# Kernel tuning notes

Hardware: AMD Instinct MI355X
Metric: run time of the kernel (lower is better)

Reference implementation:

```python
import jax, jax.numpy as jnp
import numpy as np

NUM_SCENES = 7
SHAPE = [512, 512, 256, 64]  # layer dims: 512->512->256->64
BATCH = 16384


def _xavier(key, shape):
    # nn.init.xavier_normal_ on (s, in, out): fan_in/fan_out from last two dims
    fan_in, fan_out = shape[-2], shape[-1]
    std = np.sqrt(2.0 / (fan_in + fan_out)).astype(np.float32)
    return jax.random.normal(key, shape, dtype=jnp.float32) * std


def setup_inputs() -> dict:
    key = jax.random.key(0)
    ks = jax.random.split(key, 16)
    inp = {
        "x": jax.random.normal(ks[0], (BATCH, SHAPE[0]), dtype=jnp.float32),
        "scene": jax.random.randint(ks[1], (BATCH,), 1, NUM_SCENES + 1, dtype=jnp.int64),
    }
    for i in range(3):
        din, dout = SHAPE[i], SHAPE[i + 1]
        inp[f"W{i}"] = _xavier(ks[2 + 4 * i], (NUM_SCENES, din, dout))
        inp[f"b{i}"] = jnp.zeros((NUM_SCENES, dout), dtype=jnp.float32)
        inp[f"gW{i}"] = _xavier(ks[3 + 4 * i], (1, din, dout))
        inp[f"gb{i}"] = jnp.zeros((1, dout), dtype=jnp.float32)
    return inp


def _star_linear(x, scene0, W, b, gW, gb, relu):
    # W: (S, in, out), gW: (1, in, out). Equivalent to gathering W[scene0]
    # and doing x[:,None,:] @ (w * gW), but computed as a dense GEMM over
    # all scenes followed by a per-sample select (avoids B*in*out gather).
    scaled = W * gW                                   # (S, in, out)
    out_all = jnp.einsum('bi,sio->bso', x, scaled)    # (B, S, out)
    out = jnp.take_along_axis(out_all, scene0[:, None, None], axis=1)[:, 0, :]
    out = out + b[scene0] + gb[0]
    if relu:
        out = jnp.maximum(out, 0.0)
    return out  # dropout is identity at eval


def reference(x, scene, W0, b0, gW0, gb0, W1, b1, gW1, gb1, W2, b2, gW2, gb2):
    scene0 = (scene - 1).astype(jnp.int32)
    h = _star_linear(x, scene0, W0, b0, gW0, gb0, relu=True)
    h = _star_linear(h, scene0, W1, b1, gW1, gb1, relu=True)
    h = _star_linear(h, scene0, W2, b2, gW2, gb2, relu=False)  # drop=True -> no relu
    return h
```

## Files before the change

kernel.cpp:

```cpp
#include <hip/hip_runtime.h>
#include <hip/hip_bf16.h>
#include <stdint.h>


#define BATCH   16384
#define NSCENE  7
#define TM      128
#define NBLK    (BATCH / 256)
#define MT_MAX  (BATCH / TM + NSCENE)
#define PADMAX  (BATCH + NSCENE * TM)

typedef __bf16 bf16x8 __attribute__((ext_vector_type(8)));
typedef float  f32x4  __attribute__((ext_vector_type(4)));

__device__ __forceinline__ ushort f2bf(float f) {
  union { float f; uint32_t u; } v; v.f = f;
  uint32_t r = (v.u + 0x7FFFu + ((v.u >> 16) & 1u)) >> 16;
  return (ushort)r;
}
__device__ __forceinline__ uint32_t pk2(float a, float b) {
  union { __hip_bfloat162 h; uint32_t u; } cv;
  cv.h = __float22bfloat162_rn(make_float2(a, b));
  return cv.u;
}
__device__ __forceinline__ void async16(const void* g, void* lds) {
  __builtin_amdgcn_global_load_lds(
      (const __attribute__((address_space(1))) uint32_t*)g,
      (__attribute__((address_space(3))) uint32_t*)lds, 16, 0, 0);
}

__device__ __forceinline__ void st_tile(const float* __restrict__ W,
                                        const float* __restrict__ gW,
                                        ushort* __restrict__ sT,
                                        int K, int N, int s, int n0, int k0,
                                        int tid) {
  __shared__ float tl[32][33];
  int tx = tid & 31, ty = tid >> 5;
  const float* Wp = W + (size_t)s * K * N;
#pragma unroll
  for (int i = 0; i < 4; i++) {
    int k = k0 + ty + i * 8;
    tl[ty + i * 8][tx] = Wp[(size_t)k * N + n0 + tx] * gW[(size_t)k * N + n0 + tx];
  }
  __syncthreads();
#pragma unroll
  for (int i = 0; i < 4; i++) {
    int n = n0 + ty + i * 8;
    sT[((size_t)s * N + n) * K + k0 + tx] = f2bf(tl[tx][ty + i * 8]);
  }
}

#define NB_W0 (16 * 16 * 7)
#define NB_W1 (8 * 16 * 7)
#define NB_W2 (2 * 8 * 7)
#define NB_BIAS 23
#define NB_CNT NBLK

__global__ __launch_bounds__(256) void prep_k(
    const float* __restrict__ W0, const float* __restrict__ gW0,
    const float* __restrict__ W1, const float* __restrict__ gW1,
    const float* __restrict__ W2, const float* __restrict__ gW2,
    const float* __restrict__ b0, const float* __restrict__ gb0,
    const float* __restrict__ b1, const float* __restrict__ gb1,
    const float* __restrict__ b2, const float* __restrict__ gb2,
    const int* __restrict__ scene,
    ushort* __restrict__ sT0, ushort* __restrict__ sT1, ushort* __restrict__ sT2,
    float* __restrict__ bias0, float* __restrict__ bias1, float* __restrict__ bias2,
    int* __restrict__ bcnt, int* __restrict__ rank) {
  int bid = blockIdx.x, tid = threadIdx.x;
  if (bid < NB_W0) {
    int l = bid;
    st_tile(W0, gW0, sT0, 512, 512, l / 256, (l % 16) * 32, ((l / 16) % 16) * 32, tid);
  } else if (bid < NB_W0 + NB_W1) {
    int l = bid - NB_W0;
    st_tile(W1, gW1, sT1, 512, 256, l / 128, (l % 8) * 32, ((l / 8) % 16) * 32, tid);
  } else if (bid < NB_W0 + NB_W1 + NB_W2) {
    int l = bid - NB_W0 - NB_W1;
    st_tile(W2, gW2, sT2, 256, 64, l / 16, (l % 2) * 32, ((l / 2) % 8) * 32, tid);
  } else if (bid < NB_W0 + NB_W1 + NB_W2 + NB_BIAS) {
    int t = (bid - NB_W0 - NB_W1 - NB_W2) * 256 + tid;
    if (t < 7 * 512) bias0[t] = b0[t] + gb0[t & 511];
    else if (t < 7 * 512 + 7 * 256) { int i = t - 7 * 512; bias1[i] = b1[i] + gb1[i & 255]; }
    else if (t < 7 * 512 + 7 * 256 + 7 * 64) { int i = t - 7 * 512 - 7 * 256; bias2[i] = b2[i] + gb2[i & 63]; }
  } else {
    __shared__ int l[NSCENE];
    if (tid < NSCENE) l[tid] = 0;
    __syncthreads();
    int blk = bid - NB_W0 - NB_W1 - NB_W2 - NB_BIAS;
    int i = blk * 256 + tid;
    int pos = atomicAdd(&l[scene[i] - 1], 1);
    rank[i] = pos;
    __syncthreads();
    if (tid < NSCENE) bcnt[blk * NSCENE + tid] = l[tid];
  }
}

#define PLAN_SHARED  __shared__ int sb[NBLK * NSCENE]; \
                     __shared__ int tot[NSCENE], padoff[NSCENE], cumt[NSCENE + 1];
__device__ __forceinline__ void plan_derive(const int* __restrict__ bcnt,
                                            int* sb, int* tot, int* padoff,
                                            int* cumt, int tid) {
  if (tid < NBLK * NSCENE) sb[tid] = bcnt[tid];
  if (tid + 256 < NBLK * NSCENE) sb[tid + 256] = bcnt[tid + 256];
  __syncthreads();
  if (tid < NSCENE) {
    int c = 0;
    for (int b = 0; b < NBLK; b++) c += sb[b * NSCENE + tid];
    tot[tid] = c;
  }
  __syncthreads();
  if (tid == 0) {
    int po = 0, ct = 0;
    for (int s = 0; s < NSCENE; s++) {
      padoff[s] = po; cumt[s] = ct;
      int tiles = (tot[s] + TM - 1) / TM;
      ct += tiles; po += tiles * TM;
    }
    cumt[NSCENE] = ct;
  }
  __syncthreads();
}

__global__ __launch_bounds__(256) void xc_k(const float* __restrict__ x,
                                            const int* __restrict__ scene,
                                            const int* __restrict__ rank,
                                            const int* __restrict__ bcnt,
                                            int* __restrict__ idxp,
                                            ushort* __restrict__ xc,
                                            int* __restrict__ plan_g) {
  PLAN_SHARED
  __shared__ int base7[NSCENE];
  int tid = threadIdx.x;
  plan_derive(bcnt, sb, tot, padoff, cumt, tid);
  if (blockIdx.x == 0) {
    if (tid < NSCENE) { plan_g[tid] = tot[tid]; plan_g[7 + tid] = padoff[tid]; }
    if (tid < NSCENE + 1) plan_g[14 + tid] = cumt[tid];
  }
  int myblk = blockIdx.x >> 5;
  if (tid < NSCENE) {
    int pre = 0;
    for (int b = 0; b < myblk; b++) pre += sb[b * NSCENE + tid];
    base7[tid] = padoff[tid] + pre;
  }
  __syncthreads();

  int r = blockIdx.x * 8 + (tid >> 5);
  int s = scene[r] - 1;
  int d = base7[s] + rank[r];
  if ((tid & 31) == 0) idxp[d] = r;
  int c = (tid & 31) * 16;
  const float4* p = (const float4*)(x + (size_t)r * 512 + c);
  float4 f0 = p[0], f1 = p[1], f2 = p[2], f3 = p[3];
  uint4 v0, v1;
  v0.x = pk2(f0.x, f0.y); v0.y = pk2(f0.z, f0.w);
  v0.z = pk2(f1.x, f1.y); v0.w = pk2(f1.z, f1.w);
  v1.x = pk2(f2.x, f2.y); v1.y = pk2(f2.z, f2.w);
  v1.z = pk2(f3.x, f3.y); v1.w = pk2(f3.z, f3.w);
  uint4* q = (uint4*)(xc + (size_t)d * 512 + c);
  q[0] = v0; q[1] = v1;
}

__global__ __launch_bounds__(256) void gemm0_k(
    const ushort* __restrict__ ain, const ushort* __restrict__ bw,
    const float* __restrict__ bias, const int* __restrict__ plan,
    ushort* __restrict__ hout) {
  __shared__ int splan[24];
  __shared__ __align__(16) ushort Abuf[128 * 64];
  __shared__ __align__(16) ushort Bbuf[128 * 64];

  int tid = threadIdx.x;
  if (tid < 22) splan[tid] = plan[tid];
  __syncthreads();
  const int* padoff = splan + 7;
  const int* cumt   = splan + 14;

  int t = blockIdx.x;
  if (t >= cumt[NSCENE]) return;
  int sc = 0;
  while (sc < NSCENE - 1 && t >= cumt[sc + 1]) sc++;
  int mrow0 = padoff[sc] + (t - cumt[sc]) * TM;
  int nb = blockIdx.y;

  int lane = tid & 63, wid = tid >> 6;
  int wr = wid >> 1, wc = wid & 1;

  f32x4 acc[4][4];
#pragma unroll
  for (int mt = 0; mt < 4; mt++)
#pragma unroll
    for (int nt = 0; nt < 4; nt++) acc[mt][nt] = (f32x4){0.f, 0.f, 0.f, 0.f};

  const ushort* bwS = bw + ((size_t)sc * 512 + (size_t)nb * 128) * 512;

  for (int kb = 0; kb < 8; kb++) {
#pragma unroll
    for (int i = 0; i < 4; i++) {
      int c = tid + i * 256;
      int row = c >> 3, q = c & 7;
      int kg = q ^ (row & 7);
      async16(ain + (size_t)(mrow0 + row) * 512 + kb * 64 + kg * 8,
              &Abuf[(size_t)(i * 256 + wid * 64) * 8]);
    }
#pragma unroll
    for (int i = 0; i < 4; i++) {
      int c = tid + i * 256;
      int row = c >> 3, q = c & 7;
      int kg = q ^ (row & 7);
      async16(bwS + (size_t)row * 512 + kb * 64 + kg * 8,
              &Bbuf[(size_t)(i * 256 + wid * 64) * 8]);
    }
    __syncthreads();
#pragma unroll
    for (int kk = 0; kk < 64; kk += 32) {
      bf16x8 af[4], bfr[4];
      int kc = (kk >> 3) + (lane >> 4);
#pragma unroll
      for (int mt = 0; mt < 4; mt++) {
        int row = wr * 64 + mt * 16 + (lane & 15);
        af[mt] = *(const bf16x8*)(&Abuf[(row * 8 + (kc ^ (row & 7))) * 8]);
      }
#pragma unroll
      for (int nt = 0; nt < 4; nt++) {
        int row = wc * 64 + nt * 16 + (lane & 15);
        bfr[nt] = *(const bf16x8*)(&Bbuf[(row * 8 + (kc ^ (row & 7))) * 8]);
      }
#pragma unroll
      for (int mt = 0; mt < 4; mt++)
#pragma unroll
        for (int nt = 0; nt < 4; nt++)
          acc[mt][nt] = __builtin_amdgcn_mfma_f32_16x16x32_bf16(af[mt], bfr[nt], acc[mt][nt], 0, 0, 0);
    }
    __syncthreads();
  }

#pragma unroll
  for (int mt = 0; mt < 4; mt++) {
    int rl0 = wr * 64 + mt * 16 + (lane >> 4) * 4;
#pragma unroll
    for (int nt = 0; nt < 4; nt++) {
      int col = nb * 128 + wc * 64 + nt * 16 + (lane & 15);
      float bv = bias[sc * 512 + col];
#pragma unroll
      for (int r = 0; r < 4; r++) {
        float v = fmaxf(acc[mt][nt][r] + bv, 0.f);
        hout[(size_t)(mrow0 + rl0 + r) * 512 + col] = f2bf(v);
      }
    }
  }
}

__global__ __launch_bounds__(256) void gemm12_k(
    const ushort* __restrict__ hc1, const ushort* __restrict__ sT1,
    const ushort* __restrict__ sT2, const float* __restrict__ bias1,
    const float* __restrict__ bias2, const int* __restrict__ plan,
    const int* __restrict__ idxp, float* __restrict__ out) {
  __shared__ int splan[24];
  __shared__ __align__(16) ushort Abuf[64 * 64];
  __shared__ __align__(16) ushort Bbuf[256 * 64];
  __shared__ __align__(16) ushort h2[64 * 256];

  int tid = threadIdx.x;
  if (tid < 22) splan[tid] = plan[tid];
  __syncthreads();
  const int* tot    = splan;
  const int* padoff = splan + 7;
  const int* cumt   = splan + 14;

  int j = blockIdx.x;
  int t = j >> 1;
  if (t >= cumt[NSCENE]) return;
  int sc = 0;
  while (sc < NSCENE - 1 && t >= cumt[sc + 1]) sc++;
  int mrow0 = padoff[sc] + (t - cumt[sc]) * TM + (j & 1) * 64;
  int maxloc = padoff[sc] + tot[sc];
  if (mrow0 >= maxloc) return;

  int lane = tid & 63, wid = tid >> 6;

  f32x4 acc[4][4];
#pragma unroll
  for (int mt = 0; mt < 4; mt++)
#pragma unroll
    for (int nt = 0; nt < 4; nt++) acc[mt][nt] = (f32x4){0.f, 0.f, 0.f, 0.f};

  const ushort* b1p = sT1 + (size_t)sc * 256 * 512;

  for (int kb = 0; kb < 8; kb++) {
#pragma unroll
    for (int i = 0; i < 2; i++) {
      int c = tid + i * 256;
      int row = c >> 3, q = c & 7;
      int kg = q ^ (row & 7);
      async16(hc1 + (size_t)(mrow0 + row) * 512 + kb * 64 + kg * 8,
              &Abuf[(size_t)(i * 256 + wid * 64) * 8]);
    }
#pragma unroll
    for (int i = 0; i < 8; i++) {
      int c = tid + i * 256;
      int row = c >> 3, q = c & 7;
      int kg = q ^ (row & 7);
      async16(b1p + (size_t)row * 512 + kb * 64 + kg * 8,
              &Bbuf[(size_t)(i * 256 + wid * 64) * 8]);
    }
    __syncthreads();
#pragma unroll
    for (int kk = 0; kk < 64; kk += 32) {
      bf16x8 af[4], bfr[4];
      int kc = (kk >> 3) + (lane >> 4);
#pragma unroll
      for (int mt = 0; mt < 4; mt++) {
        int row = mt * 16 + (lane & 15);
        af[mt] = *(const bf16x8*)(&Abuf[(row * 8 + (kc ^ (row & 7))) * 8]);
      }
#pragma unroll
      for (int nt = 0; nt < 4; nt++) {
        int row = wid * 64 + nt * 16 + (lane & 15);
        bfr[nt] = *(const bf16x8*)(&Bbuf[(row * 8 + (kc ^ (row & 7))) * 8]);
      }
#pragma unroll
      for (int mt = 0; mt < 4; mt++)
#pragma unroll
        for (int nt = 0; nt < 4; nt++)
          acc[mt][nt] = __builtin_amdgcn_mfma_f32_16x16x32_bf16(af[mt], bfr[nt], acc[mt][nt], 0, 0, 0);
    }
    __syncthreads();
  }

#pragma unroll
  for (int mt = 0; mt < 4; mt++) {
#pragma unroll
    for (int nt = 0; nt < 4; nt++) {
      int col = wid * 64 + nt * 16 + (lane & 15);
      float bv = bias1[sc * 256 + col];
#pragma unroll
      for (int r = 0; r < 4; r++) {
        int row = mt * 16 + (lane >> 4) * 4 + r;
        float v = fmaxf(acc[mt][nt][r] + bv, 0.f);
        h2[(row * 32 + ((col >> 3) ^ (row & 7))) * 8 + (col & 7)] = f2bf(v);
      }
    }
  }

  const ushort* b2p = sT2 + (size_t)sc * 64 * 256;
#pragma unroll
  for (int i = 0; i < 8; i++) {
    int p = tid + i * 256;
    int row = p >> 5, pc = p & 31;
    int kg = pc ^ (row & 7);
    async16(b2p + (size_t)row * 256 + kg * 8,
            &Bbuf[(size_t)(i * 256 + wid * 64) * 8]);
  }
  __syncthreads();

  f32x4 acc2[4];
#pragma unroll
  for (int nt = 0; nt < 4; nt++) acc2[nt] = (f32x4){0.f, 0.f, 0.f, 0.f};

#pragma unroll
  for (int kk = 0; kk < 256; kk += 32) {
    int kf = (kk >> 3) + (lane >> 4);
    bf16x8 af;
    {
      int row = wid * 16 + (lane & 15);
      af = *(const bf16x8*)(&h2[(row * 32 + (kf ^ (row & 7))) * 8]);
    }
    bf16x8 bfr[4];
#pragma unroll
    for (int nt = 0; nt < 4; nt++) {
      int n = nt * 16 + (lane & 15);
      bfr[nt] = *(const bf16x8*)(&Bbuf[(n * 32 + (kf ^ (n & 7))) * 8]);
    }
#pragma unroll
    for (int nt = 0; nt < 4; nt++)
      acc2[nt] = __builtin_amdgcn_mfma_f32_16x16x32_bf16(af, bfr[nt], acc2[nt], 0, 0, 0);
  }

  int rowg[4], gidx[4];
#pragma unroll
  for (int r = 0; r < 4; r++) {
    rowg[r] = mrow0 + wid * 16 + (lane >> 4) * 4 + r;
    gidx[r] = idxp[rowg[r]];
  }
#pragma unroll
  for (int nt = 0; nt < 4; nt++) {
    int col = nt * 16 + (lane & 15);
    float bv = bias2[sc * 64 + col];
#pragma unroll
    for (int r = 0; r < 4; r++) {
      if (rowg[r] < maxloc) out[(size_t)gidx[r] * 64 + col] = acc2[nt][r] + bv;
    }
  }
}

extern "C" void kernel_launch(void* const* d_in, const int* in_sizes, int n_in,
                              void* d_out, int out_size, void* d_ws, size_t ws_size,
                              hipStream_t stream) {
  const float* x   = (const float*)d_in[0];
  const int* scene = (const int*)d_in[1];
  const float* W0  = (const float*)d_in[2];
  const float* b0  = (const float*)d_in[3];
  const float* gW0 = (const float*)d_in[4];
  const float* gb0 = (const float*)d_in[5];
  const float* W1  = (const float*)d_in[6];
  const float* b1  = (const float*)d_in[7];
  const float* gW1 = (const float*)d_in[8];
  const float* gb1 = (const float*)d_in[9];
  const float* W2  = (const float*)d_in[10];
  const float* b2  = (const float*)d_in[11];
  const float* gW2 = (const float*)d_in[12];
  const float* gb2 = (const float*)d_in[13];
  float* out = (float*)d_out;

  char* ws = (char*)d_ws;
  size_t off = 0;
  auto alloc = [&](size_t bytes) -> void* {
    void* p = ws + off;
    off = (off + bytes + 255) & ~(size_t)255;
    return p;
  };
  ushort* sT0   = (ushort*)alloc((size_t)7 * 512 * 512 * 2);
  ushort* sT1   = (ushort*)alloc((size_t)7 * 256 * 512 * 2);
  ushort* sT2   = (ushort*)alloc((size_t)7 * 64 * 256 * 2);
  float*  bias0 = (float*)alloc(7 * 512 * 4);
  float*  bias1 = (float*)alloc(7 * 256 * 4);
  float*  bias2 = (float*)alloc(7 * 64 * 4);
  int*    bcnt  = (int*)alloc(NBLK * NSCENE * 4);
  int*    rank  = (int*)alloc(BATCH * 4);
  int*    idxp  = (int*)alloc(PADMAX * 4);
  int*    plan  = (int*)alloc(32 * 4);
  ushort* xc    = (ushort*)alloc((size_t)PADMAX * 512 * 2);
  ushort* hc1   = (ushort*)alloc((size_t)PADMAX * 512 * 2);
  (void)ws_size; (void)n_in; (void)in_sizes; (void)out_size;

  prep_k<<<NB_W0 + NB_W1 + NB_W2 + NB_BIAS + NB_CNT, 256, 0, stream>>>(
      W0, gW0, W1, gW1, W2, gW2, b0, gb0, b1, gb1, b2, gb2, scene,
      sT0, sT1, sT2, bias0, bias1, bias2, bcnt, rank);
  xc_k<<<BATCH / 8, 256, 0, stream>>>(x, scene, rank, bcnt, idxp, xc, plan);

  gemm0_k<<<dim3(MT_MAX, 4), 256, 0, stream>>>(xc, sT0, bias0, plan, hc1);
  gemm12_k<<<dim3(MT_MAX * 2), 256, 0, stream>>>(hc1, sT1, sT2, bias1, bias2,
                                                 plan, idxp, out);
}
```

Before: 156.6 us.

## Halve gemm0 M-tile and split fused layer1/2 kernel across N halves with atomics

gemm0 now uses 64-row M tiles instead of 128, which doubles the block count. The fused layer-1/layer-2 kernel is split across two halves of the 256-wide hidden dimension, and each half adds its partial layer-2 product into the output with atomicAdd. The output is zeroed in the gather kernel so the atomics can accumulate. The aim is more blocks and better CU occupancy on a small problem, at the cost of extra weight reloads, atomic traffic and an extra output-zeroing write.

Result: faster. 151.4 us (-3.3%).

```diff
diff --git a/kernel.cpp b/kernel.cpp
--- a/kernel.cpp
+++ b/kernel.cpp
@@ -127,10 +127,12 @@
                                             const int* __restrict__ bcnt,
                                             int* __restrict__ idxp,
                                             ushort* __restrict__ xc,
-                                            int* __restrict__ plan_g) {
+                                            int* __restrict__ plan_g,
+                                            float* __restrict__ out) {
   PLAN_SHARED
   __shared__ int base7[NSCENE];
   int tid = threadIdx.x;
+  ((float2*)out)[(size_t)blockIdx.x * 256 + tid] = make_float2(0.f, 0.f);
   plan_derive(bcnt, sb, tot, padoff, cumt, tid);
   if (blockIdx.x == 0) {
     if (tid < NSCENE) { plan_g[tid] = tot[tid]; plan_g[7 + tid] = padoff[tid]; }
@@ -165,7 +167,7 @@
     const float* __restrict__ bias, const int* __restrict__ plan,
     ushort* __restrict__ hout) {
   __shared__ int splan[24];
-  __shared__ __align__(16) ushort Abuf[128 * 64];
+  __shared__ __align__(16) ushort Abuf[64 * 64];
   __shared__ __align__(16) ushort Bbuf[128 * 64];
 
   int tid = threadIdx.x;
@@ -174,27 +176,27 @@
   const int* padoff = splan + 7;
   const int* cumt   = splan + 14;
 
-  int t = blockIdx.x;
+  int j = blockIdx.x;
+  int t = j >> 1;
   if (t >= cumt[NSCENE]) return;
   int sc = 0;
   while (sc < NSCENE - 1 && t >= cumt[sc + 1]) sc++;
-  int mrow0 = padoff[sc] + (t - cumt[sc]) * TM;
+  int mrow0 = padoff[sc] + (t - cumt[sc]) * TM + (j & 1) * 64;
   int nb = blockIdx.y;
 
   int lane = tid & 63, wid = tid >> 6;
-  int wr = wid >> 1, wc = wid & 1;
-
-  f32x4 acc[4][4];
+
+  f32x4 acc[4][2];
 #pragma unroll
   for (int mt = 0; mt < 4; mt++)
 #pragma unroll
-    for (int nt = 0; nt < 4; nt++) acc[mt][nt] = (f32x4){0.f, 0.f, 0.f, 0.f};
+    for (int nt = 0; nt < 2; nt++) acc[mt][nt] = (f32x4){0.f, 0.f, 0.f, 0.f};
 
   const ushort* bwS = bw + ((size_t)sc * 512 + (size_t)nb * 128) * 512;
 
   for (int kb = 0; kb < 8; kb++) {
 #pragma unroll
-    for (int i = 0; i < 4; i++) {
+    for (int i = 0; i < 2; i++) {
       int c = tid + i * 256;
       int row = c >> 3, q = c & 7;
       int kg = q ^ (row & 7);
@@ -212,22 +214,22 @@
     __syncthreads();
 #pragma unroll
     for (int kk = 0; kk < 64; kk += 32) {
-      bf16x8 af[4], bfr[4];
+      bf16x8 af[4], bfr[2];
       int kc = (kk >> 3) + (lane >> 4);
 #pragma unroll
       for (int mt = 0; mt < 4; mt++) {
-        int row = wr * 64 + mt * 16 + (lane & 15);
+        int row = mt * 16 + (lane & 15);
         af[mt] = *(const bf16x8*)(&Abuf[(row * 8 + (kc ^ (row & 7))) * 8]);
       }
 #pragma unroll
-      for (int nt = 0; nt < 4; nt++) {
-        int row = wc * 64 + nt * 16 + (lane & 15);
+      for (int nt = 0; nt < 2; nt++) {
+        int row = wid * 32 + nt * 16 + (lane & 15);
         bfr[nt] = *(const bf16x8*)(&Bbuf[(row * 8 + (kc ^ (row & 7))) * 8]);
       }
 #pragma unroll
       for (int mt = 0; mt < 4; mt++)
 #pragma unroll
-        for (int nt = 0; nt < 4; nt++)
+        for (int nt = 0; nt < 2; nt++)
           acc[mt][nt] = __builtin_amdgcn_mfma_f32_16x16x32_bf16(af[mt], bfr[nt], acc[mt][nt], 0, 0, 0);
     }
     __syncthreads();
@@ -235,10 +237,10 @@
 
 #pragma unroll
   for (int mt = 0; mt < 4; mt++) {
-    int rl0 = wr * 64 + mt * 16 + (lane >> 4) * 4;
-#pragma unroll
-    for (int nt = 0; nt < 4; nt++) {
-      int col = nb * 128 + wc * 64 + nt * 16 + (lane & 15);
+    int rl0 = mt * 16 + (lane >> 4) * 4;
+#pragma unroll
+    for (int nt = 0; nt < 2; nt++) {
+      int col = nb * 128 + wid * 32 + nt * 16 + (lane & 15);
       float bv = bias[sc * 512 + col];
 #pragma unroll
       for (int r = 0; r < 4; r++) {
@@ -249,15 +251,15 @@
   }
 }
 
-__global__ __launch_bounds__(256) void gemm12_k(
+__global__ __launch_bounds__(256) void gemm1_k(
     const ushort* __restrict__ hc1, const ushort* __restrict__ sT1,
     const ushort* __restrict__ sT2, const float* __restrict__ bias1,
     const float* __restrict__ bias2, const int* __restrict__ plan,
     const int* __restrict__ idxp, float* __restrict__ out) {
   __shared__ int splan[24];
   __shared__ __align__(16) ushort Abuf[64 * 64];
-  __shared__ __align__(16) ushort Bbuf[256 * 64];
-  __shared__ __align__(16) ushort h2[64 * 256];
+  __shared__ __align__(16) ushort Bbuf[128 * 64];
+  __shared__ __align__(16) ushort h2[64 * 128];
 
   int tid = threadIdx.x;
   if (tid < 22) splan[tid] = plan[tid];
@@ -274,16 +276,17 @@
   int mrow0 = padoff[sc] + (t - cumt[sc]) * TM + (j & 1) * 64;
   int maxloc = padoff[sc] + tot[sc];
   if (mrow0 >= maxloc) return;
+  int kr = blockIdx.y;
 
   int lane = tid & 63, wid = tid >> 6;
 
-  f32x4 acc[4][4];
+  f32x4 acc[4][2];
 #pragma unroll
   for (int mt = 0; mt < 4; mt++)
 #pragma unroll
-    for (int nt = 0; nt < 4; nt++) acc[mt][nt] = (f32x4){0.f, 0.f, 0.f, 0.f};
-
-  const ushort* b1p = sT1 + (size_t)sc * 256 * 512;
+    for (int nt = 0; nt < 2; nt++) acc[mt][nt] = (f32x4){0.f, 0.f, 0.f, 0.f};
+
+  const ushort* b1p = sT1 + ((size_t)sc * 256 + (size_t)kr * 128) * 512;
 
   for (int kb = 0; kb < 8; kb++) {
 #pragma unroll
@@ -295,7 +298,7 @@
               &Abuf[(size_t)(i * 256 + wid * 64) * 8]);
     }
 #pragma unroll
-    for (int i = 0; i < 8; i++) {
+    for (int i = 0; i < 4; i++) {
       int c = tid + i * 256;
       int row = c >> 3, q = c & 7;
       int kg = q ^ (row & 7);
@@ -305,7 +308,7 @@
     __syncthreads();
 #pragma unroll
     for (int kk = 0; kk < 64; kk += 32) {
-      bf16x8 af[4], bfr[4];
+      bf16x8 af[4], bfr[2];
       int kc = (kk >> 3) + (lane >> 4);
 #pragma unroll
       for (int mt = 0; mt < 4; mt++) {
@@ -313,14 +316,14 @@
         af[mt] = *(const bf16x8*)(&Abuf[(row * 8 + (kc ^ (row & 7))) * 8]);
       }
 #pragma unroll
-      for (int nt = 0; nt < 4; nt++) {
-        int row = wid * 64 + nt * 16 + (lane & 15);
+      for (int nt = 0; nt < 2; nt++) {
+        int row = wid * 32 + nt * 16 + (lane & 15);
         bfr[nt] = *(const bf16x8*)(&Bbuf[(row * 8 + (kc ^ (row & 7))) * 8]);
       }
 #pragma unroll
       for (int mt = 0; mt < 4; mt++)
 #pragma unroll
-        for (int nt = 0; nt < 4; nt++)
+        for (int nt = 0; nt < 2; nt++)
           acc[mt][nt] = __builtin_amdgcn_mfma_f32_16x16x32_bf16(af[mt], bfr[nt], acc[mt][nt], 0, 0, 0);
     }
     __syncthreads();
@@ -329,24 +332,27 @@
 #pragma unroll
   for (int mt = 0; mt < 4; mt++) {
 #pragma unroll
-    for (int nt = 0; nt < 4; nt++) {
-      int col = wid * 64 + nt * 16 + (lane & 15);
-      float bv = bias1[sc * 256 + col];
+    for (int nt = 0; nt < 2; nt++) {
+      int col = wid * 32 + nt * 16 + (lane & 15);
+      float bv = bias1[sc * 256 + kr * 128 + col];
 #pragma unroll
       for (int r = 0; r < 4; r++) {
         int row = mt * 16 + (lane >> 4) * 4 + r;
         float v = fmaxf(acc[mt][nt][r] + bv, 0.f);
-        h2[(row * 32 + ((col >> 3) ^ (row & 7))) * 8 + (col & 7)] = f2bf(v);
-      }
-    }
-  }
-
-  const ushort* b2p = sT2 + (size_t)sc * 64 * 256;
-#pragma unroll
-  for (int i = 0; i < 8; i++) {
+        int cc = col >> 3;
+        int cs = (cc & 8) | ((cc & 7) ^ (row & 7));
+        h2[(row * 16 + cs) * 8 + (col & 7)] = f2bf(v);
+      }
+    }
+  }
+  __syncthreads();
+
+  const ushort* b2p = sT2 + (size_t)sc * 64 * 256 + (size_t)kr * 128;
+#pragma unroll
+  for (int i = 0; i < 4; i++) {
     int p = tid + i * 256;
-    int row = p >> 5, pc = p & 31;
-    int kg = pc ^ (row & 7);
+    int row = p >> 4, q = p & 15;
+    int kg = (q & 8) | ((q & 7) ^ (row & 7));
     async16(b2p + (size_t)row * 256 + kg * 8,
             &Bbuf[(size_t)(i * 256 + wid * 64) * 8]);
   }
@@ -357,18 +363,20 @@
   for (int nt = 0; nt < 4; nt++) acc2[nt] = (f32x4){0.f, 0.f, 0.f, 0.f};
 
 #pragma unroll
-  for (int kk = 0; kk < 256; kk += 32) {
-    int kf = (kk >> 3) + (lane >> 4);
+  for (int kk = 0; kk < 128; kk += 32) {
+    int kc = (kk >> 3) + (lane >> 4);
     bf16x8 af;
     {
       int row = wid * 16 + (lane & 15);
-      af = *(const bf16x8*)(&h2[(row * 32 + (kf ^ (row & 7))) * 8]);
+      int ks = (kc & 8) | ((kc & 7) ^ (row & 7));
+      af = *(const bf16x8*)(&h2[(row * 16 + ks) * 8]);
     }
     bf16x8 bfr[4];
 #pragma unroll
     for (int nt = 0; nt < 4; nt++) {
       int n = nt * 16 + (lane & 15);
-      bfr[nt] = *(const bf16x8*)(&Bbuf[(n * 32 + (kf ^ (n & 7))) * 8]);
+      int ks = (kc & 8) | ((kc & 7) ^ (n & 7));
+      bfr[nt] = *(const bf16x8*)(&Bbuf[(n * 16 + ks) * 8]);
     }
 #pragma unroll
     for (int nt = 0; nt < 4; nt++)
@@ -384,10 +392,11 @@
 #pragma unroll
   for (int nt = 0; nt < 4; nt++) {
     int col = nt * 16 + (lane & 15);
-    float bv = bias2[sc * 64 + col];
+    float bv = (kr == 0) ? bias2[sc * 64 + col] : 0.f;
 #pragma unroll
     for (int r = 0; r < 4; r++) {
-      if (rowg[r] < maxloc) out[(size_t)gidx[r] * 64 + col] = acc2[nt][r] + bv;
+      if (rowg[r] < maxloc)
+        atomicAdd(&out[(size_t)gidx[r] * 64 + col], acc2[nt][r] + bv);
     }
   }
 }
@@ -435,9 +444,9 @@
   prep_k<<<NB_W0 + NB_W1 + NB_W2 + NB_BIAS + NB_CNT, 256, 0, stream>>>(
       W0, gW0, W1, gW1, W2, gW2, b0, gb0, b1, gb1, b2, gb2, scene,
       sT0, sT1, sT2, bias0, bias1, bias2, bcnt, rank);
-  xc_k<<<BATCH / 8, 256, 0, stream>>>(x, scene, rank, bcnt, idxp, xc, plan);
-
-  gemm0_k<<<dim3(MT_MAX, 4), 256, 0, stream>>>(xc, sT0, bias0, plan, hc1);
-  gemm12_k<<<dim3(MT_MAX * 2), 256, 0, stream>>>(hc1, sT1, sT2, bias1, bias2,
-                                                 plan, idxp, out);
-}
+  xc_k<<<BATCH / 8, 256, 0, stream>>>(x, scene, rank, bcnt, idxp, xc, plan, out);
+
+  gemm0_k<<<dim3(MT_MAX * 2, 4), 256, 0, stream>>>(xc, sT0, bias0, plan, hc1);
+  gemm1_k<<<dim3(MT_MAX * 2, 2), 256, 0, stream>>>(hc1, sT1, sT2, bias1, bias2,
+                                                   plan, idxp, out);
+}
```
